# Kernel tuning notes

Measured on AMD Instinct MI355X. Metric: run time of the kernel, lower is better.

Reference implementation:

```python
import jax, jax.numpy as jnp
import numpy as np
import math

D_MODEL, NHEAD, FACTOR = 1024, 16, 5
EPS = 1e-5


def layer_norm(x, g, b):
    m = jnp.mean(x, -1, keepdims=True)
    v = jnp.mean((x - m) ** 2, -1, keepdims=True)
    return (x - m) / jnp.sqrt(v + EPS) * g + b


def prob_attention(q, k, v, sample_key):
    # Informer ProbSparse causal self-attention. q,k,v: [B,H,L,E]
    B, H, L_Q, E = q.shape
    L_K = k.shape[2]
    U_part = min(FACTOR * int(np.ceil(np.log(L_K))), L_K)  # sampled keys per query
    u = min(FACTOR * int(np.ceil(np.log(L_Q))), L_Q)        # top queries kept
    idx = jax.random.randint(sample_key, (L_Q, U_part), 0, L_K)
    K_sample = k[:, :, idx, :]                               # [B,H,L_Q,U,E]
    QK_sample = jnp.einsum('bhle,bhlue->bhlu', q, K_sample)
    M = QK_sample.max(-1) - QK_sample.sum(-1) / L_K          # sparsity measure
    _, M_top = jax.lax.top_k(M, u)                           # [B,H,u] query indices
    Q_red = jnp.take_along_axis(q, M_top[..., None], axis=2) # [B,H,u,E]
    scores = jnp.einsum('bhue,bhse->bhus', Q_red, k) / math.sqrt(E)
    causal = jnp.arange(L_K)[None, None, None, :] > M_top[..., None]
    scores = jnp.where(causal, -1e9, scores)
    attn = jax.nn.softmax(scores, -1)
    upd = jnp.einsum('bhus,bhsd->bhud', attn, v)             # [B,H,u,E]
    ctx = jnp.cumsum(v, axis=2)                              # causal initial context
    b_i = jnp.arange(B)[:, None, None]
    h_i = jnp.arange(H)[None, :, None]
    return ctx.at[b_i, h_i, M_top].set(upd)


def full_attention(q, k, v):
    # q: [B,L,H,E], k,v: [B,S,H,E]; unmasked cross attention
    E = q.shape[-1]
    scores = jnp.einsum('blhe,bshe->bhls', q, k) / math.sqrt(E)
    A = jax.nn.softmax(scores, -1)
    return jnp.einsum('bhls,bshd->blhd', A, v)


def split_heads(t, B, L):
    return t.reshape(B, L, NHEAD, -1)


def decoder_layer(x, memory, sWq, sbq, sWk, sbk, sWv, sbv, sWo, sbo,
                  cWq, cbq, cWk, cbk, cWv, cbv, cWo, cbo,
                  W1, b1, W2, b2, g1, be1, g2, be2, g3, be3):
    B, L, D = x.shape
    S = memory.shape[1]
    # --- ProbSparse self-attention ---
    q = split_heads(x @ sWq + sbq, B, L).transpose(0, 2, 1, 3)
    k = split_heads(x @ sWk + sbk, B, L).transpose(0, 2, 1, 3)
    v = split_heads(x @ sWv + sbv, B, L).transpose(0, 2, 1, 3)
    ctx = prob_attention(q, k, v, jax.random.key(42))
    sa = ctx.transpose(0, 2, 1, 3).reshape(B, L, D) @ sWo + sbo
    x = layer_norm(x + sa, g1, be1)
    # --- full cross-attention ---
    q = split_heads(x @ cWq + cbq, B, L)
    k = split_heads(memory @ cWk + cbk, B, S)
    v = split_heads(memory @ cWv + cbv, B, S)
    ca = full_attention(q, k, v).reshape(B, L, D) @ cWo + cbo
    x = layer_norm(x + ca, g2, be2)
    # --- conv1d(k=1) FFN == pointwise MLP ---
    y = jax.nn.relu(x @ W1 + b1)
    y = y @ W2 + b2
    return layer_norm(x + y, g3, be3)


def setup_inputs() -> dict:
    key = jax.random.key(0)
    ks = jax.random.split(key, 32)
    D, F = D_MODEL, 4 * D_MODEL
    w = lambda k, sh: (jax.random.normal(k, sh, jnp.float32) * 0.02)
    inp = {
        'x': jax.random.normal(ks[0], (2, 2048, D), jnp.float32),
        'memory': jax.random.normal(ks[1], (2, 2048, D), jnp.float32),
    }
    names = ['sWq', 'sWk', 'sWv', 'sWo', 'cWq', 'cWk', 'cWv', 'cWo']
    for i, n in enumerate(names):
        inp[n] = w(ks[2 + i], (D, D))
        inp[n.replace('W', 'b')] = jnp.zeros((D,), jnp.float32)
    inp['W1'] = w(ks[10], (D, F)); inp['b1'] = jnp.zeros((F,), jnp.float32)
    inp['W2'] = w(ks[11], (F, D)); inp['b2'] = jnp.zeros((D,), jnp.float32)
    for i, n in enumerate(['1', '2', '3']):
        inp['g' + n] = jnp.ones((D,), jnp.float32)
        inp['be' + n] = jnp.zeros((D,), jnp.float32)
    return inp


def reference(x, memory, sWq, sbq, sWk, sbk, sWv, sbv, sWo, sbo,
              cWq, cbq, cWk, cbk, cWv, cbv, cWo, cbo,
              W1, b1, W2, b2, g1, be1, g2, be2, g3, be3):
    return decoder_layer(x, memory, sWq, sbq, sWk, sbk, sWv, sbv, sWo, sbo,
                         cWq, cbq, cWk, cbk, cWv, cbv, cWo, cbo,
                         W1, b1, W2, b2, g1, be1, g2, be2, g3, be3)
```

## Files before the change

### kernel.cpp

```cpp
#include <hip/hip_runtime.h>

static constexpr int BATCH  = 2;
static constexpr int SEQ    = 2048;
static constexpr int DMODEL = 1024;
static constexpr int NHEADS = 16;
static constexpr int EHEAD  = 64;
static constexpr int DFF    = 4096;
static constexpr int NTOP   = 40;

typedef unsigned short u16;
typedef __bf16 bf16x8_t __attribute__((ext_vector_type(8)));
typedef u16    u16x8_t  __attribute__((ext_vector_type(8)));
typedef u16    u16x4_t  __attribute__((ext_vector_type(4)));
typedef float  f32x4_t  __attribute__((ext_vector_type(4)));

static constexpr float QSCALE = 0.125f * 1.44269504088896f;
static constexpr float FIXM   = 12.0f;

static __device__ __forceinline__ u16 f2b(float f) {
  unsigned u = __builtin_bit_cast(unsigned, f);
  unsigned r = u + 0x7FFFu + ((u >> 16) & 1u);
  return (u16)(r >> 16);
}
static __device__ __forceinline__ u16 f2bf(float f) {
  __bf16 h = (__bf16)f;
  return __builtin_bit_cast(u16, h);
}
static __device__ __forceinline__ float b2f(u16 h) {
  unsigned u = ((unsigned)h) << 16;
  return __builtin_bit_cast(float, u);
}
static __device__ __forceinline__ f32x4_t mfma_bf16(u16x8_t a, u16x8_t b, f32x4_t c) {
  return __builtin_amdgcn_mfma_f32_16x16x32_bf16(
      __builtin_bit_cast(bf16x8_t, a), __builtin_bit_cast(bf16x8_t, b), c, 0, 0, 0);
}

#define GLD16(gsrc, ldst)                                                        \
  __builtin_amdgcn_global_load_lds(                                             \
      (const __attribute__((address_space(1))) void*)(gsrc),                    \
      (__attribute__((address_space(3))) void*)(ldst), 16, 0, 0)

static __device__ __forceinline__ void tf2x32(unsigned k0, unsigned k1,
                                              unsigned x0, unsigned x1,
                                              unsigned& o0, unsigned& o1) {
  unsigned ks2 = 0x1BD11BDAu ^ k0 ^ k1;
  x0 += k0; x1 += k1;
#define TFR(r) { x0 += x1; x1 = (x1 << r) | (x1 >> (32 - r)); x1 ^= x0; }
  TFR(13) TFR(15) TFR(26) TFR(6)  x0 += k1;  x1 += ks2 + 1u;
  TFR(17) TFR(29) TFR(16) TFR(24) x0 += ks2; x1 += k0 + 2u;
  TFR(13) TFR(15) TFR(26) TFR(6)  x0 += k0;  x1 += k1 + 3u;
  TFR(17) TFR(29) TFR(16) TFR(24) x0 += k1;  x1 += ks2 + 4u;
  TFR(13) TFR(15) TFR(26) TFR(6)  x0 += ks2; x1 += k0 + 5u;
#undef TFR
  o0 = x0; o1 = x1;
}

__global__ __launch_bounds__(256)
void prep_misc(const float* __restrict__ x, u16* __restrict__ xh,
               u16* __restrict__ xl, const float* __restrict__ mem,
               u16* __restrict__ memb, int* __restrict__ idx,
               const float* __restrict__ sbq, const float* __restrict__ sbk,
               float* __restrict__ biasqk, const float* __restrict__ cbk,
               const float* __restrict__ cbv, float* __restrict__ cbkv) {
  int blk = blockIdx.x, tid = threadIdx.x;
  if (blk < 4096) {
    int i = blk * 256 + tid;
    f32x4_t v = *(const f32x4_t*)(x + (size_t)i * 4);
    u16x4_t h, l;
#pragma unroll
    for (int d = 0; d < 4; ++d) {
      u16 hh = f2b(v[d]); h[d] = hh; l[d] = f2b(v[d] - b2f(hh));
    }
    *(u16x4_t*)(xh + (size_t)i * 4) = h;
    *(u16x4_t*)(xl + (size_t)i * 4) = l;
  } else if (blk < 8192) {
    int i = (blk - 4096) * 256 + tid;
    f32x4_t v = *(const f32x4_t*)(mem + (size_t)i * 4);
    u16x4_t o;
    o[0] = f2b(v[0]); o[1] = f2b(v[1]); o[2] = f2b(v[2]); o[3] = f2b(v[3]);
    *(u16x4_t*)(memb + (size_t)i * 4) = o;
  } else if (blk < 8512) {
    int i = (blk - 8192) * 256 + tid;
    unsigned c0, c1, o0, o1;
    tf2x32(0u, 42u, 0u, 1u, c0, c1);
    tf2x32(c0, c1, 0u, (unsigned)i, o0, o1);
    idx[i] = (int)((o0 ^ o1) & 2047u);
  } else {
    int i = (blk - 8512) * 256 + tid;
    if (i < 1024) biasqk[i] = sbq[i];
    else if (i < 2048) biasqk[i] = sbk[i - 1024];
    else if (i < 3072) cbkv[i - 2048] = cbk[i - 2048];
    else cbkv[i - 2048] = cbv[i - 3072];
  }
}

struct PrepW {
  const float* s2[2]; u16* dh2[2]; u16* dl2[2];
  const float* s6[6]; u16* d6[6];
  const float* W1; u16* W1T; const float* W2; u16* W2T;
};
__global__ __launch_bounds__(256)
void prep_weights(PrepW p) {
  __shared__ float t[64][65];
  int j = blockIdx.x;
  int c = threadIdx.x & 63, r4 = threadIdx.x >> 6;
  const float* in; u16* oh; u16* ol = nullptr;
  int K, N, k0, n0;
  if (j < 512) {
    int m = j >> 8, jj = j & 255;
    in = p.s2[m]; oh = p.dh2[m]; ol = p.dl2[m];
    K = 1024; N = 1024; n0 = (jj & 15) * 64; k0 = (jj >> 4) * 64;
  } else if (j < 2048) {
    int m = (j - 512) >> 8, jj = (j - 512) & 255;
    in = p.s6[m]; oh = p.d6[m];
    K = 1024; N = 1024; n0 = (jj & 15) * 64; k0 = (jj >> 4) * 64;
  } else if (j < 3072) {
    int jj = j - 2048;
    in = p.W1; oh = p.W1T;
    K = 1024; N = 4096; n0 = (jj & 63) * 64; k0 = (jj >> 6) * 64;
  } else {
    int jj = j - 3072;
    in = p.W2; oh = p.W2T;
    K = 4096; N = 1024; n0 = (jj & 15) * 64; k0 = (jj >> 4) * 64;
  }
#pragma unroll
  for (int i = 0; i < 16; ++i) {
    int r = r4 * 16 + i;
    t[r][c] = in[(size_t)(k0 + r) * N + n0 + c];
  }
  __syncthreads();
#pragma unroll
  for (int i = 0; i < 16; ++i) {
    int r = r4 * 16 + i;
    float f = t[c][r];
    u16 h = f2b(f);
    oh[(size_t)(n0 + r) * K + k0 + c] = h;
    if (ol) ol[(size_t)(n0 + r) * K + k0 + c] = f2b(f - b2f(h));
  }
}

template<int NF>
__global__ __launch_bounds__(256)
void gemm_bf(const u16* __restrict__ A, const u16* __restrict__ Bt,
             const float* __restrict__ bias, float* __restrict__ Cf,
             u16* __restrict__ Cb, int M, int N, int K, int relu) {
  __shared__ __align__(16) u16 sA[2][128 * 32];
  __shared__ __align__(16) u16 sB[2][NF * 32 * 32];
  const int tid = threadIdx.x;
  const int wave = tid >> 6, lane = tid & 63;
  const int m0 = blockIdx.x * 128, n0 = blockIdx.y * (NF * 32);
  const int wr = (wave >> 1) * 64, wc = (wave & 1) * (NF * 16);
  const int lr = lane & 15, kg = lane >> 4;
  const int wv = __builtin_amdgcn_readfirstlane(wave);

  int rowA[2], c8A[2];
#pragma unroll
  for (int rep = 0; rep < 2; ++rep) {
    int P = (rep * 256 + tid) << 4;
    int L = P ^ (((P >> 7) & 3) << 4);
    rowA[rep] = L >> 6; c8A[rep] = (L >> 4) & 3;
  }
  int rowB[NF / 2], c8B[NF / 2];
#pragma unroll
  for (int rep = 0; rep < NF / 2; ++rep) {
    int P = (rep * 256 + tid) << 4;
    int L = P ^ (((P >> 7) & 3) << 4);
    rowB[rep] = L >> 6; c8B[rep] = (L >> 4) & 3;
  }

  f32x4_t acc[4][NF];
#pragma unroll
  for (int i = 0; i < 4; ++i)
#pragma unroll
    for (int j = 0; j < NF; ++j) acc[i][j] = f32x4_t{0.f, 0.f, 0.f, 0.f};

  auto STAGE = [&](int buf, int k0) {
#pragma unroll
    for (int rep = 0; rep < 2; ++rep)
      GLD16(A + (size_t)(m0 + rowA[rep]) * K + k0 + c8A[rep] * 8,
            &sA[buf][(rep * 256 + wv * 64) * 8]);
#pragma unroll
    for (int rep = 0; rep < NF / 2; ++rep)
      GLD16(Bt + (size_t)(n0 + rowB[rep]) * K + k0 + c8B[rep] * 8,
            &sB[buf][(rep * 256 + wv * 64) * 8]);
  };

  const int nk = K >> 5;
  STAGE(0, 0);
  __syncthreads();
  for (int t = 0; t < nk; ++t) {
    const int cur = t & 1;
    if (t + 1 < nk) STAGE(cur ^ 1, (t + 1) << 5);
    u16x8_t a8[4], b8[NF];
#pragma unroll
    for (int mi = 0; mi < 4; ++mi) {
      int La = (wr + mi * 16 + lr) * 64 + kg * 16;
      a8[mi] = *(const u16x8_t*)((const char*)sA[cur] + (La ^ (((La >> 7) & 3) << 4)));
    }
#pragma unroll
    for (int ni = 0; ni < NF; ++ni) {
      int Lb = (wc + ni * 16 + lr) * 64 + kg * 16;
      b8[ni] = *(const u16x8_t*)((const char*)sB[cur] + (Lb ^ (((Lb >> 7) & 3) << 4)));
    }
#pragma unroll
    for (int mi = 0; mi < 4; ++mi)
#pragma unroll
      for (int ni = 0; ni < NF; ++ni)
        acc[mi][ni] = mfma_bf16(a8[mi], b8[ni], acc[mi][ni]);
    __syncthreads();
  }
#pragma unroll
  for (int ni = 0; ni < NF; ++ni) {
    int col = n0 + wc + ni * 16 + lr;
    float bc = bias[col];
#pragma unroll
    for (int mi = 0; mi < 4; ++mi)
#pragma unroll
      for (int r = 0; r < 4; ++r) {
        int row = m0 + wr + mi * 16 + kg * 4 + r;
        float vv = acc[mi][ni][r] + bc;
        if (relu) vv = fmaxf(vv, 0.f);
        if (Cf) Cf[(size_t)row * N + col] = vv;
        if (Cb) Cb[(size_t)row * N + col] = f2b(vv);
      }
  }
}

template<int NF>
__global__ __launch_bounds__(256)
void gemm4_bf(const u16* __restrict__ Ah, const u16* __restrict__ Al,
              const u16* __restrict__ Bh, const u16* __restrict__ Bl,
              const float* __restrict__ bias, float* __restrict__ Cf,
              int M, int N, int K) {
  __shared__ __align__(16) u16 sAh[2][128 * 32];
  __shared__ __align__(16) u16 sAl[2][128 * 32];
  __shared__ __align__(16) u16 sBh[2][NF * 32 * 32];
  __shared__ __align__(16) u16 sBl[2][NF * 32 * 32];
  const int tid = threadIdx.x;
  const int wave = tid >> 6, lane = tid & 63;
  const int m0 = blockIdx.x * 128, n0 = blockIdx.y * (NF * 32);
  const int wr = (wave >> 1) * 64, wc = (wave & 1) * (NF * 16);
  const int lr = lane & 15, kg = lane >> 4;
  const int wv = __builtin_amdgcn_readfirstlane(wave);

  int rowA[2], c8A[2];
#pragma unroll
  for (int rep = 0; rep < 2; ++rep) {
    int P = (rep * 256 + tid) << 4;
    int L = P ^ (((P >> 7) & 3) << 4);
    rowA[rep] = L >> 6; c8A[rep] = (L >> 4) & 3;
  }
  int rowB[NF / 2], c8B[NF / 2];
#pragma unroll
  for (int rep = 0; rep < NF / 2; ++rep) {
    int P = (rep * 256 + tid) << 4;
    int L = P ^ (((P >> 7) & 3) << 4);
    rowB[rep] = L >> 6; c8B[rep] = (L >> 4) & 3;
  }

  f32x4_t acc[4][NF];
#pragma unroll
  for (int i = 0; i < 4; ++i)
#pragma unroll
    for (int j = 0; j < NF; ++j) acc[i][j] = f32x4_t{0.f, 0.f, 0.f, 0.f};

  auto STAGE = [&](int buf, int k0) {
#pragma unroll
    for (int rep = 0; rep < 2; ++rep) {
      GLD16(Ah + (size_t)(m0 + rowA[rep]) * K + k0 + c8A[rep] * 8,
            &sAh[buf][(rep * 256 + wv * 64) * 8]);
      GLD16(Al + (size_t)(m0 + rowA[rep]) * K + k0 + c8A[rep] * 8,
            &sAl[buf][(rep * 256 + wv * 64) * 8]);
    }
#pragma unroll
    for (int rep = 0; rep < NF / 2; ++rep) {
      GLD16(Bh + (size_t)(n0 + rowB[rep]) * K + k0 + c8B[rep] * 8,
            &sBh[buf][(rep * 256 + wv * 64) * 8]);
      GLD16(Bl + (size_t)(n0 + rowB[rep]) * K + k0 + c8B[rep] * 8,
            &sBl[buf][(rep * 256 + wv * 64) * 8]);
    }
  };

  const int nk = K >> 5;
  STAGE(0, 0);
  __syncthreads();
  for (int t = 0; t < nk; ++t) {
    const int cur = t & 1;
    if (t + 1 < nk) STAGE(cur ^ 1, (t + 1) << 5);
    u16x8_t ah[4], al[4], bh[NF], bl[NF];
#pragma unroll
    for (int mi = 0; mi < 4; ++mi) {
      int La = (wr + mi * 16 + lr) * 64 + kg * 16;
      int off = La ^ (((La >> 7) & 3) << 4);
      ah[mi] = *(const u16x8_t*)((const char*)sAh[cur] + off);
      al[mi] = *(const u16x8_t*)((const char*)sAl[cur] + off);
    }
#pragma unroll
    for (int ni = 0; ni < NF; ++ni) {
      int Lb = (wc + ni * 16 + lr) * 64 + kg * 16;
      int off = Lb ^ (((Lb >> 7) & 3) << 4);
      bh[ni] = *(const u16x8_t*)((const char*)sBh[cur] + off);
      bl[ni] = *(const u16x8_t*)((const char*)sBl[cur] + off);
    }
#pragma unroll
    for (int mi = 0; mi < 4; ++mi)
#pragma unroll
      for (int ni = 0; ni < NF; ++ni) {
        acc[mi][ni] = mfma_bf16(ah[mi], bh[ni], acc[mi][ni]);
        acc[mi][ni] = mfma_bf16(ah[mi], bl[ni], acc[mi][ni]);
        acc[mi][ni] = mfma_bf16(al[mi], bh[ni], acc[mi][ni]);
      }
    __syncthreads();
  }
#pragma unroll
  for (int ni = 0; ni < NF; ++ni) {
    int col = n0 + wc + ni * 16 + lr;
    float bc = bias[col];
#pragma unroll
    for (int mi = 0; mi < 4; ++mi)
#pragma unroll
      for (int r = 0; r < 4; ++r) {
        int row = m0 + wr + mi * 16 + kg * 4 + r;
        Cf[(size_t)row * N + col] = acc[mi][ni][r] + bc;
      }
  }
}

__global__ __launch_bounds__(256)
void probM_kernel(const float* __restrict__ qk, const int* __restrict__ idx,
                  float* __restrict__ Mv) {
  int blk = blockIdx.x;
  int xcd = blk & 7, j = blk >> 3;
  int b = xcd >> 2;
  int part = (xcd & 3) * 128 + j;
  int l = part * 4 + (threadIdx.x >> 6);
  int lane = threadIdx.x & 63;
  const float* qrow = qk + ((size_t)b * SEQ + l) * 2048 + lane * 16;
  f32x4_t qv0 = *(const f32x4_t*)(qrow);
  f32x4_t qv1 = *(const f32x4_t*)(qrow + 4);
  f32x4_t qv2 = *(const f32x4_t*)(qrow + 8);
  f32x4_t qv3 = *(const f32x4_t*)(qrow + 12);
  const int* ip = idx + l * NTOP;
  const float* kbase = qk + (size_t)b * SEQ * 2048 + 1024 + lane * 16;
  float mmax = -3.0e38f, msum = 0.f;
  for (int pass = 0; pass < 4; ++pass) {
    int lo = pass << 9;
#pragma unroll 4
    for (int u = 0; u < NTOP; ++u) {
      int ki = ip[u];
      if ((unsigned)(ki - lo) < 512u) {
        const float* kr = kbase + (size_t)ki * 2048;
        f32x4_t k0 = *(const f32x4_t*)(kr);
        f32x4_t k1 = *(const f32x4_t*)(kr + 4);
        f32x4_t k2 = *(const f32x4_t*)(kr + 8);
        f32x4_t k3 = *(const f32x4_t*)(kr + 12);
        float p = qv0[0] * k0[0] + qv0[1] * k0[1] + qv0[2] * k0[2] + qv0[3] * k0[3]
                + qv1[0] * k1[0] + qv1[1] * k1[1] + qv1[2] * k1[2] + qv1[3] * k1[3]
                + qv2[0] * k2[0] + qv2[1] * k2[1] + qv2[2] * k2[2] + qv2[3] * k2[3]
                + qv3[0] * k3[0] + qv3[1] * k3[1] + qv3[2] * k3[2] + qv3[3] * k3[3];
        p += __shfl_xor(p, 1);
        p += __shfl_xor(p, 2);
        mmax = fmaxf(mmax, p);
        msum += p;
      }
    }
  }
  if ((lane & 3) == 0) {
    int hh = lane >> 2;
    Mv[((size_t)b * NHEADS + hh) * SEQ + l] = mmax - msum * (1.f / 2048.f);
  }
}

__global__ __launch_bounds__(256)
void topk_kernel(const float* __restrict__ Mv, int* __restrict__ Mtop) {
  int bh = blockIdx.x;
  int tid = threadIdx.x;
  int lane = tid & 63, wv = tid >> 6;
  float v8[8];
#pragma unroll
  for (int j = 0; j < 8; ++j) v8[j] = Mv[bh * 2048 + j * 256 + tid];
  __shared__ float wrv[4];
  __shared__ int wri[4];
  __shared__ int winner;
  for (int it = 0; it < NTOP; ++it) {
    float best = v8[0];
    int bj = 0;
#pragma unroll
    for (int j = 1; j < 8; ++j)
      if (v8[j] > best) { best = v8[j]; bj = j; }
    int bi = bj * 256 + tid;
#pragma unroll
    for (int m = 1; m < 64; m <<= 1) {
      float ov = __shfl_xor(best, m);
      int oi = __shfl_xor(bi, m);
      if (ov > best || (ov == best && oi < bi)) { best = ov; bi = oi; }
    }
    if (lane == 0) { wrv[wv] = best; wri[wv] = bi; }
    __syncthreads();
    if (tid == 0) {
      float bv = wrv[0]; int bbi = wri[0];
#pragma unroll
      for (int t = 1; t < 4; ++t)
        if (wrv[t] > bv || (wrv[t] == bv && wri[t] < bbi)) { bv = wrv[t]; bbi = wri[t]; }
      Mtop[bh * NTOP + it] = bbi;
      winner = bbi;
    }
    __syncthreads();
    int w = winner;
#pragma unroll
    for (int j = 0; j < 8; ++j)
      if ((w >> 8) == j && (w & 255) == tid) v8[j] = -3.4e38f;
  }
}

__global__ __launch_bounds__(256)
void kvpack_self(const float* __restrict__ qk, const u16* __restrict__ vbf,
                 u16* __restrict__ kpack, u16* __restrict__ vpack) {
  int bh = blockIdx.x, ch = blockIdx.y;
  int b = bh >> 4, hh = bh & 15;
  int tid = threadIdx.x;
  __shared__ u16 vt[64][80];
#pragma unroll
  for (int rep = 0; rep < 2; ++rep) {
    int u = rep * 256 + tid;
    int key = u >> 3, c = u & 7;
    const float* ksrc = qk + ((size_t)(b * SEQ + ch * 64 + key)) * 2048 + 1024 + hh * 64 + c * 8;
    f32x4_t k0 = *(const f32x4_t*)ksrc;
    f32x4_t k1 = *(const f32x4_t*)(ksrc + 4);
    u16x8_t d;
    d[0] = f2bf(k0[0]); d[1] = f2bf(k0[1]); d[2] = f2bf(k0[2]); d[3] = f2bf(k0[3]);
    d[4] = f2bf(k1[0]); d[5] = f2bf(k1[1]); d[6] = f2bf(k1[2]); d[7] = f2bf(k1[3]);
    int slot = (key & 3) | (((key >> 3) & 1) << 2);
    *(u16x8_t*)(kpack + ((size_t)bh * SEQ + ch * 64 + key) * 64 + ((c ^ slot) * 8)) = d;
    u16x8_t dv = *(const u16x8_t*)(vbf + ((size_t)(b * SEQ + ch * 64 + key)) * 1024 + hh * 64 + c * 8);
    *(u16x8_t*)(&vt[key][c * 8]) = dv;
  }
  __syncthreads();
#pragma unroll
  for (int rep = 0; rep < 2; ++rep) {
    int u = rep * 256 + tid;
    int e = u >> 3, c = u & 7;
    int kb = (c ^ (e & 7)) * 8;
    u16x8_t d;
#pragma unroll
    for (int j = 0; j < 8; ++j) d[j] = vt[kb + j][e];
    *(u16x8_t*)(vpack + (((size_t)bh * 32 + ch) * 64 + e) * 64 + c * 8) = d;
  }
}

__global__ __launch_bounds__(256)
void probAttn_kernel(const float* __restrict__ qk, const u16* __restrict__ kpack,
                     const u16* __restrict__ vpack, const int* __restrict__ Mtop,
                     float* __restrict__ Opart, float* __restrict__ ml) {
  const int bh = blockIdx.x, b = bh >> 4, hh = bh & 15;
  const int split = blockIdx.y;
  const int tid = threadIdx.x, wave = tid >> 6, lane = tid & 63;
  const int lr = lane & 15, kg = lane >> 4;
  const int wv = __builtin_amdgcn_readfirstlane(wave);
  __shared__ __align__(16) u16 Qs[48 * 64];
  __shared__ __align__(16) u16 Kt[2][64 * 64];
  __shared__ __align__(16) u16 Vt[2][64 * 64];

#pragma unroll
  for (int rep = 0; rep < 3; ++rep) {
    int j = tid + 256 * rep;
    int row = j >> 4, c4 = j & 15;
    int qi = Mtop[bh * NTOP + (row < NTOP ? row : NTOP - 1)];
    f32x4_t v4 = *(const f32x4_t*)(qk + ((size_t)b * SEQ + qi) * 2048 + hh * EHEAD + c4 * 4);
    u16x4_t b4;
    b4[0] = f2bf(v4[0] * QSCALE); b4[1] = f2bf(v4[1] * QSCALE);
    b4[2] = f2bf(v4[2] * QSCALE); b4[3] = f2bf(v4[3] * QSCALE);
    *(u16x4_t*)((char*)Qs + ((row * 128 + c4 * 8) ^ ((row & 7) << 4))) = b4;
  }

  const int qtile = (wave < 3) ? wave : 2;
  const int qrow_g = qtile * 16 + lr;
  const int iq = (qrow_g < NTOP) ? Mtop[bh * NTOP + qrow_g] : -1;

  int koffs[2][4], voffs[2][4], kbase16[4];
#pragma unroll
  for (int t4 = 0; t4 < 4; ++t4) {
    int arow = ((t4 >> 1) << 5) + ((lr >> 2) << 3) + ((t4 & 1) << 2) + (lr & 3);
    int slot = (arow & 3) | (((arow >> 3) & 1) << 2);
#pragma unroll
    for (int ks = 0; ks < 2; ++ks)
      koffs[ks][t4] = ((arow << 7) + (ks << 6) + (kg << 4)) ^ (slot << 4);
    kbase16[t4] = ((t4 >> 1) << 5) + (kg << 3) + ((t4 & 1) << 2);
  }
#pragma unroll
  for (int ne = 0; ne < 4; ++ne) {
    int e = ne * 16 + lr;
#pragma unroll
    for (int ks2 = 0; ks2 < 2; ++ks2)
      voffs[ks2][ne] = ((e << 7) + (ks2 << 6) + (kg << 4)) ^ ((e & 7) << 4);
  }
  const int maskbase = split * 256 - iq;

  const char* kgl = (const char*)kpack + (size_t)bh * SEQ * 128 + (size_t)split * 4 * 8192;
  const char* vgl = (const char*)vpack + (size_t)bh * 32 * 8192 + (size_t)split * 4 * 8192;
  auto STAGE = [&](int buf, int t) {
    GLD16(kgl + (size_t)t * 8192 + wv * 2048 + lane * 16, (char*)Kt[buf] + wv * 2048);
    GLD16(kgl + (size_t)t * 8192 + wv * 2048 + 1024 + lane * 16, (char*)Kt[buf] + wv * 2048 + 1024);
    GLD16(vgl + (size_t)t * 8192 + wv * 2048 + lane * 16, (char*)Vt[buf] + wv * 2048);
    GLD16(vgl + (size_t)t * 8192 + wv * 2048 + 1024 + lane * 16, (char*)Vt[buf] + wv * 2048 + 1024);
  };

  STAGE(0, 0);
  __syncthreads();

  u16x8_t bq[2];
  {
    int qrow = qtile * 16 + lr;
#pragma unroll
    for (int ks = 0; ks < 2; ++ks)
      bq[ks] = *(u16x8_t*)((char*)Qs + ((qrow * 128 + ks * 64 + kg * 16) ^ ((qrow & 7) << 4)));
  }

  f32x4_t oacc[4];
#pragma unroll
  for (int i = 0; i < 4; ++i) oacc[i] = f32x4_t{0.f, 0.f, 0.f, 0.f};
  float lsum = 0.f;

  for (int t = 0; t < 4; ++t) {
    const int cur = t & 1;
    if (t + 1 < 4) STAGE(cur ^ 1, t + 1);
    const char* kb = (const char*)Kt + cur * 8192;
    const char* vb = (const char*)Vt + cur * 8192;
    f32x4_t s[4];
#pragma unroll
    for (int i = 0; i < 4; ++i) s[i] = f32x4_t{-FIXM, -FIXM, -FIXM, -FIXM};
#pragma unroll
    for (int ks = 0; ks < 2; ++ks)
#pragma unroll
      for (int t4 = 0; t4 < 4; ++t4) {
        u16x8_t ak = *(const u16x8_t*)(kb + koffs[ks][t4]);
        s[t4] = mfma_bf16(ak, bq[ks], s[t4]);
      }
    const int mb = t * 64 + maskbase;
#pragma unroll
    for (int t4 = 0; t4 < 4; ++t4)
#pragma unroll
      for (int r = 0; r < 4; ++r)
        if (mb + kbase16[t4] + r > 0) s[t4][r] = -1e9f;
#pragma unroll
    for (int t4 = 0; t4 < 4; ++t4)
#pragma unroll
      for (int r = 0; r < 4; ++r) {
        float p = exp2f(s[t4][r]);
        s[t4][r] = p; lsum += p;
      }
#pragma unroll
    for (int ks2 = 0; ks2 < 2; ++ks2) {
      u16x8_t pa;
#pragma unroll
      for (int j = 0; j < 4; ++j) {
        pa[j] = f2bf(s[2 * ks2][j]);
        pa[4 + j] = f2bf(s[2 * ks2 + 1][j]);
      }
#pragma unroll
      for (int ne = 0; ne < 4; ++ne) {
        u16x8_t bv = *(const u16x8_t*)(vb + voffs[ks2][ne]);
        oacc[ne] = mfma_bf16(pa, bv, oacc[ne]);
      }
    }
    __syncthreads();
  }

  lsum += __shfl_xor(lsum, 16);
  lsum += __shfl_xor(lsum, 32);

  if (wave < 3) {
    float* ob = Opart + (((size_t)(bh * 8 + split)) * 48 + qtile * 16) * 64;
#pragma unroll
    for (int ne = 0; ne < 4; ++ne)
#pragma unroll
      for (int r = 0; r < 4; ++r)
        ob[(size_t)(kg * 4 + r) * 64 + ne * 16 + lr] = oacc[ne][r];
    if (kg == 0)
      ml[((size_t)(bh * 8 + split)) * 48 + qtile * 16 + lr] = lsum;
  }
}

__global__ __launch_bounds__(64)
void probCombine_kernel(const float* __restrict__ Opart, const float* __restrict__ ml,
                        const int* __restrict__ Mtop, u16* __restrict__ ctxb) {
  int bh = blockIdx.x / NTOP, q = blockIdx.x % NTOP;
  int e = threadIdx.x;
  int b = bh >> 4, hh = bh & 15;
  float lstar = 0.f, acc = 0.f;
#pragma unroll
  for (int s = 0; s < 8; ++s) {
    lstar += ml[((size_t)(bh * 8 + s)) * 48 + q];
    acc += Opart[(((size_t)(bh * 8 + s)) * 48 + q) * 64 + e];
  }
  int row = Mtop[bh * NTOP + q];
  ctxb[((size_t)b * SEQ + row) * DMODEL + hh * EHEAD + e] = f2bf(acc / lstar);
}

__global__ __launch_bounds__(64)
void scanA_kernel(const u16* __restrict__ v, float* __restrict__ csum) {
  int bh = blockIdx.x, ch = blockIdx.y;
  int b = bh >> 4, hh = bh & 15, e = threadIdx.x;
  size_t base = ((size_t)b * SEQ + ch * 128) * DMODEL + hh * EHEAD + e;
  float run = 0.f;
  for (int i = 0; i < 128; ++i) run += b2f(v[base + (size_t)i * DMODEL]);
  csum[(bh * 16 + ch) * 64 + e] = run;
}
__global__ __launch_bounds__(64)
void scanB_kernel(const u16* __restrict__ v, const float* __restrict__ csum,
                  u16* __restrict__ ctxb) {
  int bh = blockIdx.x, ch = blockIdx.y;
  int b = bh >> 4, hh = bh & 15, e = threadIdx.x;
  float run = 0.f;
  for (int cc = 0; cc < ch; ++cc) run += csum[(bh * 16 + cc) * 64 + e];
  size_t base = ((size_t)b * SEQ + ch * 128) * DMODEL + hh * EHEAD + e;
  for (int i = 0; i < 128; ++i) {
    run += b2f(v[base + (size_t)i * DMODEL]);
    ctxb[base + (size_t)i * DMODEL] = f2bf(run);
  }
}

__global__ __launch_bounds__(256)
void kvpack_kernel(const u16* __restrict__ kv, u16* __restrict__ kpack,
                   u16* __restrict__ vpack) {
  int bh = blockIdx.x, ch = blockIdx.y;
  int b = bh >> 4, hh = bh & 15;
  int tid = threadIdx.x;
  __shared__ u16 vt[64][80];
#pragma unroll
  for (int rep = 0; rep < 2; ++rep) {
    int u = rep * 256 + tid;
    int key = u >> 3, c = u & 7;
    u16x8_t d = *(const u16x8_t*)(kv + ((size_t)(b * SEQ + ch * 64 + key)) * 2048 + hh * 64 + c * 8);
    int slot = (key & 3) | (((key >> 3) & 1) << 2);
    *(u16x8_t*)(kpack + ((size_t)bh * SEQ + ch * 64 + key) * 64 + ((c ^ slot) * 8)) = d;
    u16x8_t dv = *(const u16x8_t*)(kv + ((size_t)(b * SEQ + ch * 64 + key)) * 2048 + 1024 + hh * 64 + c * 8);
    *(u16x8_t*)(&vt[key][c * 8]) = dv;
  }
  __syncthreads();
#pragma unroll
  for (int rep = 0; rep < 2; ++rep) {
    int u = rep * 256 + tid;
    int e = u >> 3, c = u & 7;
    int kb = (c ^ (e & 7)) * 8;
    u16x8_t d;
#pragma unroll
    for (int j = 0; j < 8; ++j) d[j] = vt[kb + j][e];
    *(u16x8_t*)(vpack + (((size_t)bh * 32 + ch) * 64 + e) * 64 + c * 8) = d;
  }
}

__global__ __launch_bounds__(512)
void cross_attn_kernel(const float* __restrict__ q2, const u16* __restrict__ kpack,
                       const u16* __restrict__ vpack, u16* __restrict__ cab) {
  const int bh = blockIdx.x, b = bh >> 4, hh = bh & 15;
  const int qt0 = blockIdx.y * 128;
  const int tid = threadIdx.x, wave = tid >> 6, lane = tid & 63;
  const int lr = lane & 15, kg = lane >> 4;
  const int wv = __builtin_amdgcn_readfirstlane(wave);
  __shared__ __align__(16) u16 Qs[128 * 64];
  __shared__ __align__(16) u16 Kt[2][64 * 64];
  __shared__ __align__(16) u16 Vt[2][64 * 64];

#pragma unroll
  for (int i = 0; i < 4; ++i) {
    int j = tid + 512 * i;
    int row = j >> 4, c4 = j & 15;
    f32x4_t v4 = *(const f32x4_t*)(q2 + ((size_t)b * SEQ + qt0 + row) * DMODEL + hh * EHEAD + c4 * 4);
    u16x4_t b4;
    b4[0] = f2bf(v4[0] * QSCALE); b4[1] = f2bf(v4[1] * QSCALE);
    b4[2] = f2bf(v4[2] * QSCALE); b4[3] = f2bf(v4[3] * QSCALE);
    *(u16x4_t*)((char*)Qs + ((row * 128 + c4 * 8) ^ ((row & 7) << 4))) = b4;
  }

  int koffs[2][4], voffs[2][4];
#pragma unroll
  for (int t4 = 0; t4 < 4; ++t4) {
    int arow = ((t4 >> 1) << 5) + ((lr >> 2) << 3) + ((t4 & 1) << 2) + (lr & 3);
    int slot = (arow & 3) | (((arow >> 3) & 1) << 2);
#pragma unroll
    for (int ks = 0; ks < 2; ++ks)
      koffs[ks][t4] = ((arow << 7) + (ks << 6) + (kg << 4)) ^ (slot << 4);
  }
#pragma unroll
  for (int ne = 0; ne < 4; ++ne) {
    int e = ne * 16 + lr;
#pragma unroll
    for (int ks2 = 0; ks2 < 2; ++ks2)
      voffs[ks2][ne] = ((e << 7) + (ks2 << 6) + (kg << 4)) ^ ((e & 7) << 4);
  }

  const char* kgl = (const char*)kpack + (size_t)bh * SEQ * 128;
  const char* vgl = (const char*)vpack + (size_t)bh * 32 * 8192;
  auto STAGE = [&](int buf, int t) {
    GLD16(kgl + (size_t)t * 8192 + wv * 1024 + lane * 16, (char*)Kt[buf] + wv * 1024);
    GLD16(vgl + (size_t)t * 8192 + wv * 1024 + lane * 16, (char*)Vt[buf] + wv * 1024);
  };

  STAGE(0, 0);
  __syncthreads();

  u16x8_t bq[2];
  {
    int qrow = wave * 16 + lr;
#pragma unroll
    for (int ks = 0; ks < 2; ++ks)
      bq[ks] = *(u16x8_t*)((char*)Qs + ((qrow * 128 + ks * 64 + kg * 16) ^ ((qrow & 7) << 4)));
  }

  f32x4_t oacc[4];
#pragma unroll
  for (int i = 0; i < 4; ++i) oacc[i] = f32x4_t{0.f, 0.f, 0.f, 0.f};
  float lsum = 0.f;

  for (int t = 0; t < 32; ++t) {
    const int cur = t & 1;
    if (t + 1 < 32) STAGE(cur ^ 1, t + 1);
    const char* kb = (const char*)Kt + cur * 8192;
    const char* vb = (const char*)Vt + cur * 8192;
    f32x4_t s[4];
#pragma unroll
    for (int i = 0; i < 4; ++i) s[i] = f32x4_t{-FIXM, -FIXM, -FIXM, -FIXM};
#pragma unroll
    for (int ks = 0; ks < 2; ++ks)
#pragma unroll
      for (int t4 = 0; t4 < 4; ++t4) {
        u16x8_t ak = *(const u16x8_t*)(kb + koffs[ks][t4]);
        s[t4] = mfma_bf16(ak, bq[ks], s[t4]);
      }
#pragma unroll
    for (int t4 = 0; t4 < 4; ++t4)
#pragma unroll
      for (int r = 0; r < 4; ++r) {
        float p = exp2f(s[t4][r]);
        s[t4][r] = p; lsum += p;
      }
#pragma unroll
    for (int ks2 = 0; ks2 < 2; ++ks2) {
      u16x8_t pa;
#pragma unroll
      for (int j = 0; j < 4; ++j) {
        pa[j] = f2bf(s[2 * ks2][j]);
        pa[4 + j] = f2bf(s[2 * ks2 + 1][j]);
      }
#pragma unroll
      for (int ne = 0; ne < 4; ++ne) {
        u16x8_t bv = *(const u16x8_t*)(vb + voffs[ks2][ne]);
        oacc[ne] = mfma_bf16(pa, bv, oacc[ne]);
      }
    }
    __syncthreads();
  }

  lsum += __shfl_xor(lsum, 16);
  lsum += __shfl_xor(lsum, 32);
  float inv4[4];
#pragma unroll
  for (int r = 0; r < 4; ++r) inv4[r] = 1.0f / __shfl(lsum, kg * 4 + r);
#pragma unroll
  for (int ne = 0; ne < 4; ++ne)
#pragma unroll
    for (int r = 0; r < 4; ++r) {
      int row = qt0 + wave * 16 + kg * 4 + r;
      int col = hh * EHEAD + ne * 16 + lr;
      cab[((size_t)b * SEQ + row) * DMODEL + col] = f2bf(oacc[ne][r] * inv4[r]);
    }
}

__global__ __launch_bounds__(256)
void ln_kernel(const float* __restrict__ x, const float* __restrict__ r,
               const float* __restrict__ g, const float* __restrict__ be,
               float* __restrict__ outf, u16* __restrict__ outb) {
  int row = blockIdx.x, tid = threadIdx.x;
  size_t base = (size_t)row * DMODEL;
  float v[4];
  float s = 0.f, sq = 0.f;
#pragma unroll
  for (int i = 0; i < 4; ++i) {
    int c = tid + i * 256;
    float t = x[base + c] + r[base + c];
    v[i] = t; s += t; sq += t * t;
  }
  __shared__ float rs[256], rq[256];
  rs[tid] = s; rq[tid] = sq;
  __syncthreads();
  for (int st = 128; st > 0; st >>= 1) {
    if (tid < st) { rs[tid] += rs[tid + st]; rq[tid] += rq[tid + st]; }
    __syncthreads();
  }
  float mean = rs[0] * (1.f / DMODEL);
  float var = rq[0] * (1.f / DMODEL) - mean * mean;
  float rstd = rsqrtf(var + 1e-5f);
#pragma unroll
  for (int i = 0; i < 4; ++i) {
    int c = tid + i * 256;
    float o = (v[i] - mean) * rstd * g[c] + be[c];
    if (outf) outf[base + c] = o;
    if (outb) outb[base + c] = f2bf(o);
  }
}

static inline void gemm(const u16* A, const u16* Bt, const float* bias, float* Cf,
                        u16* Cb, int M, int N, int K, int relu, hipStream_t s,
                        int big = 0) {
  if (big)
    gemm_bf<4><<<dim3(M / 128, N / 128), 256, 0, s>>>(A, Bt, bias, Cf, Cb, M, N, K, relu);
  else
    gemm_bf<2><<<dim3(M / 128, N / 64), 256, 0, s>>>(A, Bt, bias, Cf, Cb, M, N, K, relu);
}
static inline void gemm4(const u16* Ah, const u16* Al, const u16* Bh, const u16* Bl,
                         const float* bias, float* Cf, int M, int N, int K, hipStream_t s) {
  gemm4_bf<4><<<dim3(M / 128, N / 128), 256, 0, s>>>(Ah, Al, Bh, Bl, bias, Cf, M, N, K);
}

extern "C" void kernel_launch(void* const* d_in, const int* in_sizes, int n_in,
                              void* d_out, int out_size, void* d_ws, size_t ws_size,
                              hipStream_t stream) {
  const float* x   = (const float*)d_in[0];
  const float* mem = (const float*)d_in[1];
  const float* sWq = (const float*)d_in[2];  const float* sbq = (const float*)d_in[3];
  const float* sWk = (const float*)d_in[4];  const float* sbk = (const float*)d_in[5];
  const float* sWv = (const float*)d_in[6];  const float* sbv = (const float*)d_in[7];
  const float* sWo = (const float*)d_in[8];  const float* sbo = (const float*)d_in[9];
  const float* cWq = (const float*)d_in[10]; const float* cbq = (const float*)d_in[11];
  const float* cWk = (const float*)d_in[12]; const float* cbk = (const float*)d_in[13];
  const float* cWv = (const float*)d_in[14]; const float* cbv = (const float*)d_in[15];
  const float* cWo = (const float*)d_in[16]; const float* cbo = (const float*)d_in[17];
  const float* W1  = (const float*)d_in[18]; const float* b1  = (const float*)d_in[19];
  const float* W2  = (const float*)d_in[20]; const float* b2  = (const float*)d_in[21];
  const float* g1  = (const float*)d_in[22]; const float* be1 = (const float*)d_in[23];
  const float* g2  = (const float*)d_in[24]; const float* be2 = (const float*)d_in[25];
  const float* g3  = (const float*)d_in[26]; const float* be3 = (const float*)d_in[27];
  float* outp = (float*)d_out;
  char* ws = (char*)d_ws;
  const size_t MB = 1ull << 20;

  int*   idx    = (int*)(ws);
  float* Mv     = (float*)(ws + 0x60000);
  int*   Mtop   = (int*)(ws + 0xA0000);
  float* biasqk = (float*)(ws + 0x120000);
  float* cbkv   = (float*)(ws + 0x122000);
  float* csum   = (float*)(ws + 0x130000);

  u16* WqkhT = (u16*)(ws + 2 * MB);
  u16* WqklT = (u16*)(ws + 6 * MB);
  u16* sWvT  = (u16*)(ws + 10 * MB);
  u16* sWoT  = (u16*)(ws + 12 * MB);
  u16* cWqT  = (u16*)(ws + 14 * MB);
  u16* cWkvT = (u16*)(ws + 16 * MB);
  u16* cWoT  = (u16*)(ws + 20 * MB);
  u16* W1T   = (u16*)(ws + 22 * MB);
  u16* W2T   = (u16*)(ws + 30 * MB);

  u16* xh   = (u16*)(ws + 38 * MB);
  u16* xl   = (u16*)(ws + 46 * MB);
  u16* memb = (u16*)(ws + 54 * MB);

  float* qk    = (float*)(ws + 62 * MB);
  u16*   vbf   = (u16*)(ws + 94 * MB);
  u16*   kpks  = (u16*)(ws + 102 * MB);
  u16*   vpks  = (u16*)(ws + 46 * MB);
  float* Opart = (float*)(ws + 110 * MB);
  float* mlbuf = (float*)(ws + 113 * MB);
  u16*   ctxb  = (u16*)(ws + 78 * MB);
  float* sa    = (float*)(ws + 94 * MB);
  float* x1    = (float*)(ws + 62 * MB);
  u16*   x1b   = (u16*)(ws + 78 * MB);
  float* q2    = (float*)(ws + 94 * MB);
  u16*   kv2b  = (u16*)(ws + 38 * MB);
  u16*   kpk   = (u16*)(ws + 54 * MB);
  u16*   vpk   = (u16*)(ws + 110 * MB);
  u16*   cab   = (u16*)(ws + 38 * MB);
  float* ca2   = (float*)(ws + 94 * MB);
  float* x2    = (float*)(ws + 38 * MB);
  u16*   x2b   = (u16*)(ws + 54 * MB);
  u16*   hbb   = (u16*)(ws + 62 * MB);
  float* yb    = (float*)(ws + 94 * MB);

  const int MROWS = BATCH * SEQ;

  prep_misc<<<8528, 256, 0, stream>>>(x, xh, xl, mem, memb, idx,
                                      sbq, sbk, biasqk, cbk, cbv, cbkv);
  {
    PrepW p;
    p.s2[0] = sWq; p.dh2[0] = WqkhT;               p.dl2[0] = WqklT;
    p.s2[1] = sWk; p.dh2[1] = WqkhT + 1024 * 1024; p.dl2[1] = WqklT + 1024 * 1024;
    p.s6[0] = sWv; p.d6[0] = sWvT;
    p.s6[1] = sWo; p.d6[1] = sWoT;
    p.s6[2] = cWq; p.d6[2] = cWqT;
    p.s6[3] = cWk; p.d6[3] = cWkvT;
    p.s6[4] = cWv; p.d6[4] = cWkvT + 1024 * 1024;
    p.s6[5] = cWo; p.d6[5] = cWoT;
    p.W1 = W1; p.W1T = W1T; p.W2 = W2; p.W2T = W2T;
    prep_weights<<<4096, 256, 0, stream>>>(p);
  }

  gemm4(xh, xl, WqkhT, WqklT, biasqk, qk, MROWS, 2048, DMODEL, stream);
  gemm(xh, sWvT, sbv, nullptr, vbf, MROWS, DMODEL, DMODEL, 0, stream);
  probM_kernel<<<BATCH * SEQ / 4, 256, 0, stream>>>(qk, idx, Mv);
  topk_kernel<<<BATCH * NHEADS, 256, 0, stream>>>(Mv, Mtop);
  kvpack_self<<<dim3(BATCH * NHEADS, SEQ / 64), 256, 0, stream>>>(qk, vbf, kpks, vpks);
  probAttn_kernel<<<dim3(BATCH * NHEADS, 8), 256, 0, stream>>>(qk, kpks, vpks, Mtop, Opart, mlbuf);
  scanA_kernel<<<dim3(BATCH * NHEADS, 16), 64, 0, stream>>>(vbf, csum);
  scanB_kernel<<<dim3(BATCH * NHEADS, 16), 64, 0, stream>>>(vbf, csum, ctxb);
  probCombine_kernel<<<BATCH * NHEADS * NTOP, 64, 0, stream>>>(Opart, mlbuf, Mtop, ctxb);
  gemm(ctxb, sWoT, sbo, sa, nullptr, MROWS, DMODEL, DMODEL, 0, stream);
  ln_kernel<<<MROWS, 256, 0, stream>>>(x, sa, g1, be1, x1, x1b);

  gemm(x1b, cWqT, cbq, q2, nullptr, MROWS, DMODEL, DMODEL, 0, stream);
  gemm(memb, cWkvT, cbkv, nullptr, kv2b, MROWS, 2048, DMODEL, 0, stream, 1);
  kvpack_kernel<<<dim3(BATCH * NHEADS, SEQ / 64), 256, 0, stream>>>(kv2b, kpk, vpk);
  cross_attn_kernel<<<dim3(BATCH * NHEADS, SEQ / 128), 512, 0, stream>>>(q2, kpk, vpk, cab);
  gemm(cab, cWoT, cbo, ca2, nullptr, MROWS, DMODEL, DMODEL, 0, stream);
  ln_kernel<<<MROWS, 256, 0, stream>>>(x1, ca2, g2, be2, x2, x2b);

  gemm(x2b, W1T, b1, nullptr, hbb, MROWS, DFF, DMODEL, 1, stream, 1);
  gemm(hbb, W2T, b2, yb, nullptr, MROWS, DMODEL, DFF, 0, stream);
  ln_kernel<<<MROWS, 256, 0, stream>>>(x2, yb, g3, be3, outp, nullptr);
}
```

Before: 535.3 us.

## Split-K the cross-attn output and FFN down-projection GEMMs, sum partials in LayerNorm

Adds a split-K GEMM kernel that divides K into two halves along grid z, writing two fp32 partial outputs. The previous 128x64-tile GEMM for cWo and W2 is replaced with 128x128 tiles and two K-halves, and a new three-input LayerNorm kernel sums the residual and both partials. The aim is more parallel blocks and shorter per-block K loops for the long-K W2 GEMM. The cost is an extra 16MB fp32 partial write and read per GEMM, plus a new workspace region at offset 2MB that could alias other buffers.

Result: no change. 526.9 us, median of 2 (-1.6%).

```diff
diff --git a/kernel.cpp b/kernel.cpp
--- a/kernel.cpp
+++ b/kernel.cpp
@@ -222,6 +222,95 @@
         if (relu) vv = fmaxf(vv, 0.f);
         if (Cf) Cf[(size_t)row * N + col] = vv;
         if (Cb) Cb[(size_t)row * N + col] = f2b(vv);
+      }
+  }
+}
+
+template<int NF>
+__global__ __launch_bounds__(256)
+void gemm_ks(const u16* __restrict__ A, const u16* __restrict__ Bt,
+             const float* __restrict__ bias, float* __restrict__ C0,
+             float* __restrict__ C1, int M, int N, int K) {
+  __shared__ __align__(16) u16 sA[2][128 * 32];
+  __shared__ __align__(16) u16 sB[2][NF * 32 * 32];
+  const int tid = threadIdx.x;
+  const int wave = tid >> 6, lane = tid & 63;
+  const int m0 = blockIdx.x * 128, n0 = blockIdx.y * (NF * 32);
+  const int zz = blockIdx.z;
+  const int Kh = K >> 1;
+  const u16* Ab = A + (size_t)zz * Kh;
+  const u16* Bb = Bt + (size_t)zz * Kh;
+  float* Cf = zz ? C1 : C0;
+  const int wr = (wave >> 1) * 64, wc = (wave & 1) * (NF * 16);
+  const int lr = lane & 15, kg = lane >> 4;
+  const int wv = __builtin_amdgcn_readfirstlane(wave);
+
+  int rowA[2], c8A[2];
+#pragma unroll
+  for (int rep = 0; rep < 2; ++rep) {
+    int P = (rep * 256 + tid) << 4;
+    int L = P ^ (((P >> 7) & 3) << 4);
+    rowA[rep] = L >> 6; c8A[rep] = (L >> 4) & 3;
+  }
+  int rowB[NF / 2], c8B[NF / 2];
+#pragma unroll
+  for (int rep = 0; rep < NF / 2; ++rep) {
+    int P = (rep * 256 + tid) << 4;
+    int L = P ^ (((P >> 7) & 3) << 4);
+    rowB[rep] = L >> 6; c8B[rep] = (L >> 4) & 3;
+  }
+
+  f32x4_t acc[4][NF];
+#pragma unroll
+  for (int i = 0; i < 4; ++i)
+#pragma unroll
+    for (int j = 0; j < NF; ++j) acc[i][j] = f32x4_t{0.f, 0.f, 0.f, 0.f};
+
+  auto STAGE = [&](int buf, int k0) {
+#pragma unroll
+    for (int rep = 0; rep < 2; ++rep)
+      GLD16(Ab + (size_t)(m0 + rowA[rep]) * K + k0 + c8A[rep] * 8,
+            &sA[buf][(rep * 256 + wv * 64) * 8]);
+#pragma unroll
+    for (int rep = 0; rep < NF / 2; ++rep)
+      GLD16(Bb + (size_t)(n0 + rowB[rep]) * K + k0 + c8B[rep] * 8,
+            &sB[buf][(rep * 256 + wv * 64) * 8]);
+  };
+
+  const int nk = Kh >> 5;
+  STAGE(0, 0);
+  __syncthreads();
+  for (int t = 0; t < nk; ++t) {
+    const int cur = t & 1;
+    if (t + 1 < nk) STAGE(cur ^ 1, (t + 1) << 5);
+    u16x8_t a8[4], b8[NF];
+#pragma unroll
+    for (int mi = 0; mi < 4; ++mi) {
+      int La = (wr + mi * 16 + lr) * 64 + kg * 16;
+      a8[mi] = *(const u16x8_t*)((const char*)sA[cur] + (La ^ (((La >> 7) & 3) << 4)));
+    }
+#pragma unroll
+    for (int ni = 0; ni < NF; ++ni) {
+      int Lb = (wc + ni * 16 + lr) * 64 + kg * 16;
+      b8[ni] = *(const u16x8_t*)((const char*)sB[cur] + (Lb ^ (((Lb >> 7) & 3) << 4)));
+    }
+#pragma unroll
+    for (int mi = 0; mi < 4; ++mi)
+#pragma unroll
+      for (int ni = 0; ni < NF; ++ni)
+        acc[mi][ni] = mfma_bf16(a8[mi], b8[ni], acc[mi][ni]);
+    __syncthreads();
+  }
+#pragma unroll
+  for (int ni = 0; ni < NF; ++ni) {
+    int col = n0 + wc + ni * 16 + lr;
+    float bc = (zz == 0) ? bias[col] : 0.f;
+#pragma unroll
+    for (int mi = 0; mi < 4; ++mi)
+#pragma unroll
+      for (int r = 0; r < 4; ++r) {
+        int row = m0 + wr + mi * 16 + kg * 4 + r;
+        Cf[(size_t)row * N + col] = acc[mi][ni][r] + bc;
       }
   }
 }
@@ -800,6 +889,40 @@
   }
 }
 
+__global__ __launch_bounds__(256)
+void ln3_kernel(const float* __restrict__ x, const float* __restrict__ r0,
+                const float* __restrict__ r1, const float* __restrict__ g,
+                const float* __restrict__ be, float* __restrict__ outf,
+                u16* __restrict__ outb) {
+  int row = blockIdx.x, tid = threadIdx.x;
+  size_t base = (size_t)row * DMODEL;
+  float v[4];
+  float s = 0.f, sq = 0.f;
+#pragma unroll
+  for (int i = 0; i < 4; ++i) {
+    int c = tid + i * 256;
+    float t = x[base + c] + r0[base + c] + r1[base + c];
+    v[i] = t; s += t; sq += t * t;
+  }
+  __shared__ float rs[256], rq[256];
+  rs[tid] = s; rq[tid] = sq;
+  __syncthreads();
+  for (int st = 128; st > 0; st >>= 1) {
+    if (tid < st) { rs[tid] += rs[tid + st]; rq[tid] += rq[tid + st]; }
+    __syncthreads();
+  }
+  float mean = rs[0] * (1.f / DMODEL);
+  float var = rq[0] * (1.f / DMODEL) - mean * mean;
+  float rstd = rsqrtf(var + 1e-5f);
+#pragma unroll
+  for (int i = 0; i < 4; ++i) {
+    int c = tid + i * 256;
+    float o = (v[i] - mean) * rstd * g[c] + be[c];
+    if (outf) outf[base + c] = o;
+    if (outb) outb[base + c] = f2bf(o);
+  }
+}
+
 static inline void gemm(const u16* A, const u16* Bt, const float* bias, float* Cf,
                         u16* Cb, int M, int N, int K, int relu, hipStream_t s,
                         int big = 0) {
@@ -807,6 +930,10 @@
     gemm_bf<4><<<dim3(M / 128, N / 128), 256, 0, s>>>(A, Bt, bias, Cf, Cb, M, N, K, relu);
   else
     gemm_bf<2><<<dim3(M / 128, N / 64), 256, 0, s>>>(A, Bt, bias, Cf, Cb, M, N, K, relu);
+}
+static inline void gemmks(const u16* A, const u16* Bt, const float* bias, float* C0,
+                          float* C1, int M, int N, int K, hipStream_t s) {
+  gemm_ks<4><<<dim3(M / 128, N / 128, 2), 256, 0, s>>>(A, Bt, bias, C0, C1, M, N, K);
 }
 static inline void gemm4(const u16* Ah, const u16* Al, const u16* Bh, const u16* Bl,
                          const float* bias, float* Cf, int M, int N, int K, hipStream_t s) {
@@ -871,11 +998,13 @@
   u16*   kpk   = (u16*)(ws + 54 * MB);
   u16*   vpk   = (u16*)(ws + 110 * MB);
   u16*   cab   = (u16*)(ws + 38 * MB);
-  float* ca2   = (float*)(ws + 94 * MB);
+  float* ca0   = (float*)(ws + 94 * MB);
+  float* ca1   = (float*)(ws + 2 * MB);
   float* x2    = (float*)(ws + 38 * MB);
   u16*   x2b   = (u16*)(ws + 54 * MB);
   u16*   hbb   = (u16*)(ws + 62 * MB);
-  float* yb    = (float*)(ws + 94 * MB);
+  float* yb0   = (float*)(ws + 94 * MB);
+  float* yb1   = (float*)(ws + 2 * MB);
 
   const int MROWS = BATCH * SEQ;
 
@@ -911,10 +1040,10 @@
   gemm(memb, cWkvT, cbkv, nullptr, kv2b, MROWS, 2048, DMODEL, 0, stream, 1);
   kvpack_kernel<<<dim3(BATCH * NHEADS, SEQ / 64), 256, 0, stream>>>(kv2b, kpk, vpk);
   cross_attn_kernel<<<dim3(BATCH * NHEADS, SEQ / 128), 512, 0, stream>>>(q2, kpk, vpk, cab);
-  gemm(cab, cWoT, cbo, ca2, nullptr, MROWS, DMODEL, DMODEL, 0, stream);
-  ln_kernel<<<MROWS, 256, 0, stream>>>(x1, ca2, g2, be2, x2, x2b);
+  gemmks(cab, cWoT, cbo, ca0, ca1, MROWS, DMODEL, DMODEL, stream);
+  ln3_kernel<<<MROWS, 256, 0, stream>>>(x1, ca0, ca1, g2, be2, x2, x2b);
 
   gemm(x2b, W1T, b1, nullptr, hbb, MROWS, DFF, DMODEL, 1, stream, 1);
-  gemm(hbb, W2T, b2, yb, nullptr, MROWS, DMODEL, DFF, 0, stream);
-  ln_kernel<<<MROWS, 256, 0, stream>>>(x2, yb, g3, be3, outp, nullptr);
-}
+  gemmks(hbb, W2T, b2, yb0, yb1, MROWS, DMODEL, DFF, stream);
+  ln3_kernel<<<MROWS, 256, 0, stream>>>(x2, yb0, yb1, g3, be3, outp, nullptr);
+}
```
